# Optimization experiments

Measured on AMD Instinct MI355X. Metric: run time of the kernel, lower is better.

Reference implementation:

```python
import jax, jax.numpy as jnp
import numpy as np

B, DIM, H, W = 4, 512, 64, 64
NH = 8
HD = DIM // NH  # 64
CS = 16         # TTT mini_batch_size
BASE_LR = 1.0
EPS_IN = 1e-6   # inner ttt LayerNorm / post_norm eps
EPS_OUT = 1e-5  # wrapper nn.LayerNorm eps


def _ln(x, g, b, eps):
    mu = x.mean(-1, keepdims=True)
    var = ((x - mu) ** 2).mean(-1, keepdims=True)
    return (x - mu) / jnp.sqrt(var + eps) * g + b


def _ln_l2_bwd(Z, tgt, g, b):
    # fused: d/dZ of 0.5*||LN(Z; g,b) - tgt||^2
    D = Z.shape[-1]
    mu = Z.mean(-1, keepdims=True)
    var = ((Z - mu) ** 2).mean(-1, keepdims=True)
    std = jnp.sqrt(var + EPS_IN)
    xh = (Z - mu) / std
    gxh = ((g * xh + b) - tgt) * g
    return (D * gxh - gxh.sum(-1, keepdims=True) - xh * (gxh * xh).sum(-1, keepdims=True)) / (D * std)


def _rope(x, L):
    # x: [B, nh, L, f], llama-style rotary, theta=10000
    inv = 1.0 / (10000.0 ** (jnp.arange(0, HD, 2, dtype=jnp.float32) / HD))
    fr = jnp.arange(L, dtype=jnp.float32)[:, None] * inv[None, :]
    emb = jnp.concatenate([fr, fr], axis=-1)  # [L, f]
    cos, sin = jnp.cos(emb), jnp.sin(emb)
    x1, x2 = jnp.split(x, 2, axis=-1)
    return x * cos + jnp.concatenate([-x2, x1], axis=-1) * sin


def setup_inputs() -> dict:
    key = jax.random.key(0)
    ks = jax.random.split(key, 8)
    r = lambda k, s: 0.02 * jax.random.normal(k, s, dtype=jnp.float32)
    return {
        "x": jax.random.normal(ks[0], (B, DIM, H, W), dtype=jnp.float32),
        "ln_w": jnp.ones((DIM,), jnp.float32), "ln_b": jnp.zeros((DIM,), jnp.float32),
        "q_w": r(ks[1], (DIM, DIM)), "k_w": r(ks[2], (DIM, DIM)),
        "v_w": r(ks[3], (DIM, DIM)), "o_w": r(ks[4], (DIM, DIM)),
        "W1": r(ks[5], (NH, HD, HD)), "b1": jnp.zeros((NH, 1, HD), jnp.float32),
        "ttt_ln_w": jnp.ones((NH, HD), jnp.float32), "ttt_ln_b": jnp.zeros((NH, HD), jnp.float32),
        "lr_w": r(ks[6], (NH, 1, DIM)), "lr_b": jnp.zeros((NH, 1, 1), jnp.float32),
        "tok_idx_delta": jnp.zeros((CS,), jnp.float32),
        "post_w": jnp.ones((DIM,), jnp.float32), "post_b": jnp.zeros((DIM,), jnp.float32),
    }


def _ttt_linear(xn, q_w, k_w, v_w, o_w, W1, b1, ttt_ln_w, ttt_ln_b, lr_w, lr_b, tok_idx_delta, post_w, post_b):
    Bsz, L, _ = xn.shape
    NC = L // CS
    heads = lambda t: t.reshape(Bsz, L, NH, HD).transpose(0, 2, 1, 3)  # [B,nh,L,f]
    XQ = _rope(heads(xn @ q_w.T), L)
    XK = _rope(heads(xn @ k_w.T), L)
    XV = heads(xn @ v_w.T)

    # per-token learning rates eta: [B,nh,NC,CS,CS]
    Xc = xn.reshape(Bsz, NC, CS, DIM)
    ttt_lr = jax.nn.sigmoid(jnp.einsum("bnkc,hdc->bhnkd", Xc, lr_w) + lr_b.reshape(1, NH, 1, 1, 1))
    ttt_lr_eta = (BASE_LR / HD) * ttt_lr.transpose(0, 1, 2, 4, 3)  # [B,nh,NC,1,CS]
    token_idx = jnp.maximum(1.0 / jnp.arange(1, CS + 1, dtype=jnp.float32) + tok_idx_delta, 0.0)
    eta = token_idx.reshape(1, 1, 1, CS, 1) * ttt_lr_eta  # [B,nh,NC,CS,CS]

    g = ttt_ln_w[None, :, None, :]   # [1,nh,1,f]
    bb = ttt_ln_b[None, :, None, :]

    def step(carry, inp):
        W1c, b1c = carry                       # [B,nh,f,f], [B,nh,1,f]
        xq, xk, xv, et = inp                   # [B,nh,CS,f], eta [B,nh,CS,CS]
        Z1 = xk @ W1c + b1c
        grad = _ln_l2_bwd(Z1, xv - xk, g, bb)  # [B,nh,CS,f]
        Attn1 = jnp.tril(xq @ xk.swapaxes(-1, -2))
        b1_bar = b1c - jnp.tril(et) @ grad
        Z1_bar = xq @ W1c - (et * Attn1) @ grad + b1_bar
        last_eta = et[..., -1, :, None]        # [B,nh,CS,1]
        W1n = W1c - (last_eta * xk).swapaxes(-1, -2) @ grad
        b1n = b1c - (last_eta * grad).sum(-2, keepdims=True)
        return (W1n, b1n), xq + _ln(Z1_bar, g, bb, EPS_IN)

    W1_0 = jnp.broadcast_to(W1[None], (Bsz, NH, HD, HD)) + 0.0
    b1_0 = jnp.broadcast_to(b1[None], (Bsz, NH, 1, HD)) + 0.0
    chunk = lambda t: t.reshape(Bsz, NH, NC, CS, HD).transpose(2, 0, 1, 3, 4)
    _, out = jax.lax.scan(step, (W1_0, b1_0),
                          (chunk(XQ), chunk(XK), chunk(XV), eta.transpose(2, 0, 1, 3, 4)))
    # [NC,B,nh,CS,f] -> [B,L,D]
    out = out.transpose(1, 2, 0, 3, 4).reshape(Bsz, NH, L, HD).transpose(0, 2, 1, 3).reshape(Bsz, L, DIM)
    return _ln(out, post_w, post_b, EPS_IN) @ o_w.T


def reference(x, ln_w, ln_b, q_w, k_w, v_w, o_w, W1, b1, ttt_ln_w, ttt_ln_b, lr_w, lr_b, tok_idx_delta, post_w, post_b):
    Bsz, d = x.shape[:2]
    n_tok = x.shape[2] * x.shape[3]
    xf = x.reshape(Bsz, d, n_tok).transpose(0, 2, 1)   # [B, L, D]
    xn = _ln(xf, ln_w, ln_b, EPS_OUT)
    y = _ttt_linear(xn, q_w, k_w, v_w, o_w, W1, b1, ttt_ln_w, ttt_ln_b, lr_w, lr_b, tok_idx_delta, post_w, post_b)
    return y.transpose(0, 2, 1).reshape(x.shape)
```

## Files before the change

kernel.cpp:

```cpp
#include <hip/hip_runtime.h>
#include <hip/hip_bf16.h>
#include <math.h>

#define L_TOK 4096
#define DIMC  512

static __device__ __forceinline__ float4 f4fma(float a, const float4 b, const float4 c) {
    return make_float4(fmaf(a, b.x, c.x), fmaf(a, b.y, c.y), fmaf(a, b.z, c.z), fmaf(a, b.w, c.w));
}

__global__ __launch_bounds__(256) void rope_table_kernel(float* __restrict__ ctab, float* __restrict__ stab) {
    int idx = blockIdx.x * 256 + threadIdx.x;
    if (idx >= L_TOK * 32) return;
    int t = idx >> 5, m = idx & 31;
    float inv = 1.0f / powf(10000.0f, (float)(2 * m) * (1.0f / 64.0f));
    float fr = (float)t * inv;
    ctab[idx] = cosf(fr);
    stab[idx] = sinf(fr);
}

__global__ __launch_bounds__(256) void ln_in_kernel(const float* __restrict__ x,
                                                    const float* __restrict__ w,
                                                    const float* __restrict__ bia,
                                                    float* __restrict__ xn) {
    __shared__ float tile[16][516];
    __shared__ float redA[4][16], redB[4][16];
    __shared__ float mu_s[16], rs_s[16];
    int blk = blockIdx.x;
    int b = blk >> 8;
    int t0 = (blk & 255) << 4;
    int tid = threadIdx.x;
    int tt = tid & 15, cg = tid >> 4;
    int wid = tid >> 6;
    const float* xp = x + (size_t)b * DIMC * L_TOK + t0 + tt;
    float sum = 0.0f, sq = 0.0f;
#pragma unroll
    for (int i = 0; i < 32; i++) {
        int c = cg + (i << 4);
        float v = xp[(size_t)c * L_TOK];
        tile[tt][c] = v;
        sum += v; sq += v * v;
    }
    sum += __shfl_xor(sum, 16); sum += __shfl_xor(sum, 32);
    sq  += __shfl_xor(sq, 16);  sq  += __shfl_xor(sq, 32);
    if ((tid & 63) < 16) { redA[wid][tt] = sum; redB[wid][tt] = sq; }
    __syncthreads();
    if (tid < 16) {
        float s = redA[0][tid] + redA[1][tid] + redA[2][tid] + redA[3][tid];
        float q = redB[0][tid] + redB[1][tid] + redB[2][tid] + redB[3][tid];
        float mu = s * (1.0f / 512.0f);
        mu_s[tid] = mu;
        rs_s[tid] = rsqrtf(q * (1.0f / 512.0f) - mu * mu + 1e-5f);
    }
    __syncthreads();
    int half = tid >> 7;
    int cc = (tid & 127) << 2;
    float4 wv = *(const float4*)&w[cc];
    float4 bv = *(const float4*)&bia[cc];
    float* xnp = xn + ((size_t)b * L_TOK + t0) * DIMC;
#pragma unroll
    for (int i = 0; i < 8; i++) {
        int rr = half + (i << 1);
        float mu = mu_s[rr], rs = rs_s[rr];
        float4 v = *(float4*)&tile[rr][cc];
        float4 o;
        o.x = fmaf((v.x - mu) * rs, wv.x, bv.x);
        o.y = fmaf((v.y - mu) * rs, wv.y, bv.y);
        o.z = fmaf((v.z - mu) * rs, wv.z, bv.z);
        o.w = fmaf((v.w - mu) * rs, wv.w, bv.w);
        *(float4*)&xnp[(size_t)rr * DIMC + cc] = o;
    }
}

__global__ __launch_bounds__(256) void lr_kernel(const float* __restrict__ xn,
                                                 const float* __restrict__ lrw,
                                                 const float* __restrict__ lrb,
                                                 float* __restrict__ lre) {
    int tid = threadIdx.x;
    int lane = tid & 63, wid = tid >> 6;
    int tok = blockIdx.x * 4 + wid;
    const float* xp = xn + (size_t)tok * DIMC + lane * 8;
    float4 a0 = *(const float4*)xp;
    float4 a1 = *(const float4*)(xp + 4);
    int bb = tok >> 12, t = tok & 4095;
#pragma unroll
    for (int h = 0; h < 8; h++) {
        const float* wp = lrw + h * DIMC + lane * 8;
        float4 w0 = *(const float4*)wp;
        float4 w1 = *(const float4*)(wp + 4);
        float s = a0.x * w0.x + a0.y * w0.y + a0.z * w0.z + a0.w * w0.w
                + a1.x * w1.x + a1.y * w1.y + a1.z * w1.z + a1.w * w1.w;
        s += __shfl_xor(s, 1); s += __shfl_xor(s, 2); s += __shfl_xor(s, 4);
        s += __shfl_xor(s, 8); s += __shfl_xor(s, 16); s += __shfl_xor(s, 32);
        if (lane == 0) {
            float v = s + lrb[h];
            lre[(size_t)(bb * 8 + h) * L_TOK + t] = (1.0f / 64.0f) / (1.0f + expf(-v));
        }
    }
}

__global__ __launch_bounds__(256) void qkv_gemm_kernel(const float* __restrict__ A,
                                                       const float* __restrict__ qw,
                                                       const float* __restrict__ kw,
                                                       const float* __restrict__ vw,
                                                       float* __restrict__ XQ,
                                                       float* __restrict__ XK,
                                                       float* __restrict__ XV) {
    __shared__ float As[16][68];
    __shared__ float Bs[16][68];
    int tid = threadIdx.x;
    int mt = blockIdx.x, nt = blockIdx.y;
    const float* wsel = (nt < 8) ? qw : (nt < 16) ? kw : vw;
    int h = nt & 7;
    int lrow = tid >> 2, lk = (tid & 3) << 2;
    int tm = tid >> 4, tn = tid & 15;
    float acc[4][4] = {};
    const float* ap = A + (size_t)(mt * 64 + lrow) * DIMC + lk;
    const float* bp = wsel + (size_t)(h * 64 + lrow) * DIMC + lk;
    for (int k0 = 0; k0 < DIMC; k0 += 16) {
        float4 av = *(const float4*)(ap + k0);
        float4 bv = *(const float4*)(bp + k0);
        As[lk + 0][lrow] = av.x; As[lk + 1][lrow] = av.y; As[lk + 2][lrow] = av.z; As[lk + 3][lrow] = av.w;
        Bs[lk + 0][lrow] = bv.x; Bs[lk + 1][lrow] = bv.y; Bs[lk + 2][lrow] = bv.z; Bs[lk + 3][lrow] = bv.w;
        __syncthreads();
#pragma unroll
        for (int kk = 0; kk < 16; kk++) {
            float4 a = *(const float4*)&As[kk][tm << 2];
            float4 bq = *(const float4*)&Bs[kk][tn << 2];
            float aa[4] = {a.x, a.y, a.z, a.w};
            float bb[4] = {bq.x, bq.y, bq.z, bq.w};
#pragma unroll
            for (int i = 0; i < 4; i++)
#pragma unroll
                for (int j = 0; j < 4; j++)
                    acc[i][j] = fmaf(aa[i], bb[j], acc[i][j]);
        }
        __syncthreads();
    }
    int m0 = mt * 64 + (tm << 2);
    int bb2 = m0 >> 12, t = m0 & 4095;
    float* dst = (nt < 8) ? XQ : (nt < 16) ? XK : XV;
    dst += ((size_t)(bb2 * 8 + h) * L_TOK + t) * 64 + (tn << 2);
#pragma unroll
    for (int i = 0; i < 4; i++)
        *(float4*)(dst + (size_t)i * 64) = make_float4(acc[i][0], acc[i][1], acc[i][2], acc[i][3]);
}

__global__ __launch_bounds__(256) void rope_kernel(float* __restrict__ XQ, float* __restrict__ XK,
                                                   const float* __restrict__ ctab,
                                                   const float* __restrict__ stab) {
    int idx = blockIdx.x * 256 + threadIdx.x;
    int d = idx & 31;
    int t = (idx >> 5) & 4095;
    int bh = (idx >> 17) & 31;
    int tensor = idx >> 22;
    float* p = (tensor ? XK : XQ) + ((size_t)bh * L_TOK + t) * 64;
    float c = ctab[(t << 5) + d], s = stab[(t << 5) + d];
    float x1 = p[d], x2 = p[d + 32];
    p[d] = x1 * c - x2 * s;
    p[d + 32] = x2 * c + x1 * s;
}

__global__ __launch_bounds__(256) void scan_kernel(const float* __restrict__ XQ,
                                                   const float* __restrict__ XK,
                                                   const float* __restrict__ XV,
                                                   const float* __restrict__ lre,
                                                   const float* __restrict__ tok_delta,
                                                   const float* __restrict__ W1i,
                                                   const float* __restrict__ b1i,
                                                   const float* __restrict__ tw,
                                                   const float* __restrict__ tb,
                                                   float* __restrict__ attn_out) {
    __shared__ float W1[64][64];
    __shared__ float b1v[64];
    __shared__ float xqs[2][16][68], xks[2][16][68], xvs[2][16][68];
    __shared__ float grads[16][68];
    __shared__ float etas[2][16];
    __shared__ float coefC[16][16];
    __shared__ float sj[16];
    int tid = threadIdx.x;
    int r = tid >> 4, dq = tid & 15, d0 = dq << 2;
    int bh = blockIdx.x, h = bh & 7, b = bh >> 3;
#pragma unroll
    for (int i = 0; i < 4; i++) {
        int c = r + (i << 4);
        *(float4*)&W1[c][d0] = *(const float4*)&W1i[(size_t)h * 4096 + c * 64 + d0];
    }
    if (r == 0) *(float4*)&b1v[d0] = *(const float4*)&b1i[h * 64 + d0];
    float4 gw = *(const float4*)&tw[h * 64 + d0];
    float4 bw = *(const float4*)&tb[h * 64 + d0];
    float tok_r = fmaxf(1.0f / (float)(r + 1) + tok_delta[r], 0.0f);
    float tok15 = fmaxf(1.0f / 16.0f + tok_delta[15], 0.0f);
    const size_t base = (size_t)bh * L_TOK * 64;
    {
        size_t off = base + (size_t)r * 64 + d0;
        *(float4*)&xqs[0][r][d0] = *(const float4*)(XQ + off);
        *(float4*)&xks[0][r][d0] = *(const float4*)(XK + off);
        *(float4*)&xvs[0][r][d0] = *(const float4*)(XV + off);
        if (tid < 16) etas[0][tid] = lre[(size_t)bh * L_TOK + tid];
    }
    __syncthreads();
    int cur = 0;
    for (int n = 0; n < 256; n++) {
        int np = (n < 255) ? n + 1 : 255;
        size_t poff = base + (size_t)np * 1024 + (size_t)r * 64 + d0;
        float4 pfq = *(const float4*)(XQ + poff);
        float4 pfk = *(const float4*)(XK + poff);
        float4 pfv = *(const float4*)(XV + poff);
        float pfe = 0.0f;
        if (tid < 16) pfe = lre[(size_t)bh * L_TOK + np * 16 + tid];

        float4 z = *(float4*)&b1v[d0];
        float att = 0.0f;
#pragma unroll
        for (int c4 = 0; c4 < 16; c4++) {
            int c = c4 << 2;
            float4 xkr = *(float4*)&xks[cur][r][c];
            float4 xqr = *(float4*)&xqs[cur][r][c];
            float4 xkq = *(float4*)&xks[cur][dq][c];
            att += xqr.x * xkq.x + xqr.y * xkq.y + xqr.z * xkq.z + xqr.w * xkq.w;
            z = f4fma(xkr.x, *(float4*)&W1[c + 0][d0], z);
            z = f4fma(xkr.y, *(float4*)&W1[c + 1][d0], z);
            z = f4fma(xkr.z, *(float4*)&W1[c + 2][d0], z);
            z = f4fma(xkr.w, *(float4*)&W1[c + 3][d0], z);
        }
        float s = z.x + z.y + z.z + z.w;
        s += __shfl_xor(s, 1); s += __shfl_xor(s, 2); s += __shfl_xor(s, 4); s += __shfl_xor(s, 8);
        float mu = s * (1.0f / 64.0f);
        float4 dz = make_float4(z.x - mu, z.y - mu, z.z - mu, z.w - mu);
        float q = dz.x * dz.x + dz.y * dz.y + dz.z * dz.z + dz.w * dz.w;
        q += __shfl_xor(q, 1); q += __shfl_xor(q, 2); q += __shfl_xor(q, 4); q += __shfl_xor(q, 8);
        float rstd = rsqrtf(q * (1.0f / 64.0f) + 1e-6f);
        float4 xh = make_float4(dz.x * rstd, dz.y * rstd, dz.z * rstd, dz.w * rstd);
        float4 xvv = *(float4*)&xvs[cur][r][d0];
        float4 xkk = *(float4*)&xks[cur][r][d0];
        float4 gxh;
        gxh.x = (fmaf(gw.x, xh.x, bw.x) - (xvv.x - xkk.x)) * gw.x;
        gxh.y = (fmaf(gw.y, xh.y, bw.y) - (xvv.y - xkk.y)) * gw.y;
        gxh.z = (fmaf(gw.z, xh.z, bw.z) - (xvv.z - xkk.z)) * gw.z;
        gxh.w = (fmaf(gw.w, xh.w, bw.w) - (xvv.w - xkk.w)) * gw.w;
        float s1 = gxh.x + gxh.y + gxh.z + gxh.w;
        s1 += __shfl_xor(s1, 1); s1 += __shfl_xor(s1, 2); s1 += __shfl_xor(s1, 4); s1 += __shfl_xor(s1, 8);
        float s2 = gxh.x * xh.x + gxh.y * xh.y + gxh.z * xh.z + gxh.w * xh.w;
        s2 += __shfl_xor(s2, 1); s2 += __shfl_xor(s2, 2); s2 += __shfl_xor(s2, 4); s2 += __shfl_xor(s2, 8);
        float cgr = rstd * (1.0f / 64.0f);
        float4 grad;
        grad.x = (64.0f * gxh.x - s1 - xh.x * s2) * cgr;
        grad.y = (64.0f * gxh.y - s1 - xh.y * s2) * cgr;
        grad.z = (64.0f * gxh.z - s1 - xh.z * s2) * cgr;
        grad.w = (64.0f * gxh.w - s1 - xh.w * s2) * cgr;
        *(float4*)&grads[r][d0] = grad;
        float ceta = etas[cur][dq];
        coefC[r][dq] = (dq <= r) ? tok_r * ceta * (1.0f + att) : 0.0f;
        if (r == 15) sj[dq] = tok15 * ceta;
        __syncthreads();

        float4 z2 = *(float4*)&b1v[d0];
#pragma unroll
        for (int c4 = 0; c4 < 16; c4++) {
            int c = c4 << 2;
            float4 xqr = *(float4*)&xqs[cur][r][c];
            z2 = f4fma(xqr.x, *(float4*)&W1[c + 0][d0], z2);
            z2 = f4fma(xqr.y, *(float4*)&W1[c + 1][d0], z2);
            z2 = f4fma(xqr.z, *(float4*)&W1[c + 2][d0], z2);
            z2 = f4fma(xqr.w, *(float4*)&W1[c + 3][d0], z2);
        }
#pragma unroll
        for (int j = 0; j < 16; j++) {
            float cj = coefC[r][j];
            float4 gj = *(float4*)&grads[j][d0];
            z2 = f4fma(-cj, gj, z2);
        }
        float so = z2.x + z2.y + z2.z + z2.w;
        so += __shfl_xor(so, 1); so += __shfl_xor(so, 2); so += __shfl_xor(so, 4); so += __shfl_xor(so, 8);
        float mu2 = so * (1.0f / 64.0f);
        float4 dz2 = make_float4(z2.x - mu2, z2.y - mu2, z2.z - mu2, z2.w - mu2);
        float q2 = dz2.x * dz2.x + dz2.y * dz2.y + dz2.z * dz2.z + dz2.w * dz2.w;
        q2 += __shfl_xor(q2, 1); q2 += __shfl_xor(q2, 2); q2 += __shfl_xor(q2, 4); q2 += __shfl_xor(q2, 8);
        float rstd2 = rsqrtf(q2 * (1.0f / 64.0f) + 1e-6f);
        float4 xq4 = *(float4*)&xqs[cur][r][d0];
        float4 o;
        o.x = fmaf(dz2.x * rstd2, gw.x, bw.x) + xq4.x;
        o.y = fmaf(dz2.y * rstd2, gw.y, bw.y) + xq4.y;
        o.z = fmaf(dz2.z * rstd2, gw.z, bw.z) + xq4.z;
        o.w = fmaf(dz2.w * rstd2, gw.w, bw.w) + xq4.w;
        *(float4*)(attn_out + ((size_t)b * L_TOK + (size_t)n * 16 + r) * DIMC + h * 64 + d0) = o;
        __syncthreads();

        float4 acc0 = make_float4(0, 0, 0, 0), acc1 = acc0, acc2 = acc0, acc3 = acc0;
#pragma unroll
        for (int j = 0; j < 16; j++) {
            float sjj = sj[j];
            float4 gj = *(float4*)&grads[j][d0];
            acc0 = f4fma(sjj * xks[cur][j][r],      gj, acc0);
            acc1 = f4fma(sjj * xks[cur][j][r + 16], gj, acc1);
            acc2 = f4fma(sjj * xks[cur][j][r + 32], gj, acc2);
            acc3 = f4fma(sjj * xks[cur][j][r + 48], gj, acc3);
        }
        {
            float4 w0 = *(float4*)&W1[r][d0];
            w0.x -= acc0.x; w0.y -= acc0.y; w0.z -= acc0.z; w0.w -= acc0.w;
            *(float4*)&W1[r][d0] = w0;
            float4 w1 = *(float4*)&W1[r + 16][d0];
            w1.x -= acc1.x; w1.y -= acc1.y; w1.z -= acc1.z; w1.w -= acc1.w;
            *(float4*)&W1[r + 16][d0] = w1;
            float4 w2 = *(float4*)&W1[r + 32][d0];
            w2.x -= acc2.x; w2.y -= acc2.y; w2.z -= acc2.z; w2.w -= acc2.w;
            *(float4*)&W1[r + 32][d0] = w2;
            float4 w3 = *(float4*)&W1[r + 48][d0];
            w3.x -= acc3.x; w3.y -= acc3.y; w3.z -= acc3.z; w3.w -= acc3.w;
            *(float4*)&W1[r + 48][d0] = w3;
        }
        if (r == 0) {
            float4 ab = make_float4(0, 0, 0, 0);
#pragma unroll
            for (int j = 0; j < 16; j++)
                ab = f4fma(sj[j], *(float4*)&grads[j][d0], ab);
            float4 bv = *(float4*)&b1v[d0];
            bv.x -= ab.x; bv.y -= ab.y; bv.z -= ab.z; bv.w -= ab.w;
            *(float4*)&b1v[d0] = bv;
        }
        *(float4*)&xqs[cur ^ 1][r][d0] = pfq;
        *(float4*)&xks[cur ^ 1][r][d0] = pfk;
        *(float4*)&xvs[cur ^ 1][r][d0] = pfv;
        if (tid < 16) etas[cur ^ 1][tid] = pfe;
        __syncthreads();
        cur ^= 1;
    }
}

__global__ __launch_bounds__(256) void post_ln_kernel(float* __restrict__ at,
                                                      const float* __restrict__ w,
                                                      const float* __restrict__ b) {
    __shared__ float redA[4], redB[4];
    int row = blockIdx.x, tid = threadIdx.x;
    float* p = at + (size_t)row * DIMC;
    float v0 = p[tid], v1 = p[tid + 256];
    float s = v0 + v1, q = v0 * v0 + v1 * v1;
    s += __shfl_xor(s, 1); s += __shfl_xor(s, 2); s += __shfl_xor(s, 4);
    s += __shfl_xor(s, 8); s += __shfl_xor(s, 16); s += __shfl_xor(s, 32);
    q += __shfl_xor(q, 1); q += __shfl_xor(q, 2); q += __shfl_xor(q, 4);
    q += __shfl_xor(q, 8); q += __shfl_xor(q, 16); q += __shfl_xor(q, 32);
    if ((tid & 63) == 0) { redA[tid >> 6] = s; redB[tid >> 6] = q; }
    __syncthreads();
    s = redA[0] + redA[1] + redA[2] + redA[3];
    q = redB[0] + redB[1] + redB[2] + redB[3];
    float mu = s * (1.0f / 512.0f);
    float rs = rsqrtf(q * (1.0f / 512.0f) - mu * mu + 1e-6f);
    p[tid]       = fmaf((v0 - mu) * rs, w[tid],       b[tid]);
    p[tid + 256] = fmaf((v1 - mu) * rs, w[tid + 256], b[tid + 256]);
}

__global__ __launch_bounds__(256) void out_gemm_kernel(const float* __restrict__ A,
                                                       const float* __restrict__ ow,
                                                       float* __restrict__ out) {
    __shared__ float As[16][68];
    __shared__ float Bs[16][68];
    int tid = threadIdx.x;
    int mt = blockIdx.x, nt = blockIdx.y;
    int lrow = tid >> 2, lk = (tid & 3) << 2;
    int tm = tid >> 4, tn = tid & 15;
    float acc[4][4] = {};
    const float* ap = A + (size_t)(mt * 64 + lrow) * DIMC + lk;
    const float* bp = ow + (size_t)(nt * 64 + lrow) * DIMC + lk;
    for (int k0 = 0; k0 < DIMC; k0 += 16) {
        float4 av = *(const float4*)(ap + k0);
        float4 bv = *(const float4*)(bp + k0);
        As[lk + 0][lrow] = av.x; As[lk + 1][lrow] = av.y; As[lk + 2][lrow] = av.z; As[lk + 3][lrow] = av.w;
        Bs[lk + 0][lrow] = bv.x; Bs[lk + 1][lrow] = bv.y; Bs[lk + 2][lrow] = bv.z; Bs[lk + 3][lrow] = bv.w;
        __syncthreads();
#pragma unroll
        for (int kk = 0; kk < 16; kk++) {
            float4 a = *(const float4*)&As[kk][tm << 2];
            float4 bq = *(const float4*)&Bs[kk][tn << 2];
            float aa[4] = {a.x, a.y, a.z, a.w};
            float bb[4] = {bq.x, bq.y, bq.z, bq.w};
#pragma unroll
            for (int i = 0; i < 4; i++)
#pragma unroll
                for (int j = 0; j < 4; j++)
                    acc[i][j] = fmaf(aa[i], bb[j], acc[i][j]);
        }
        __syncthreads();
    }
    int m0 = mt * 64 + (tm << 2);
    int bb2 = m0 >> 12, t = m0 & 4095;
    int n0 = nt * 64 + (tn << 2);
#pragma unroll
    for (int j = 0; j < 4; j++)
        *(float4*)(out + ((size_t)(bb2 * DIMC) + n0 + j) * L_TOK + t) =
            make_float4(acc[0][j], acc[1][j], acc[2][j], acc[3][j]);
}

extern "C" void kernel_launch(void* const* d_in, const int* in_sizes, int n_in,
                              void* d_out, int out_size, void* d_ws, size_t ws_size,
                              hipStream_t stream) {
    (void)in_sizes; (void)n_in; (void)out_size; (void)ws_size;
    const float* x       = (const float*)d_in[0];
    const float* ln_w    = (const float*)d_in[1];
    const float* ln_b    = (const float*)d_in[2];
    const float* q_w     = (const float*)d_in[3];
    const float* k_w     = (const float*)d_in[4];
    const float* v_w     = (const float*)d_in[5];
    const float* o_w     = (const float*)d_in[6];
    const float* W1      = (const float*)d_in[7];
    const float* b1      = (const float*)d_in[8];
    const float* ttt_w   = (const float*)d_in[9];
    const float* ttt_b   = (const float*)d_in[10];
    const float* lr_w    = (const float*)d_in[11];
    const float* lr_b    = (const float*)d_in[12];
    const float* tok_d   = (const float*)d_in[13];
    const float* post_w  = (const float*)d_in[14];
    const float* post_b  = (const float*)d_in[15];

    float* ws = (float*)d_ws;
    const size_t NTD = (size_t)4 * L_TOK * DIMC;
    float* xn   = ws;
    float* XQb  = ws + NTD;
    float* XKb  = ws + 2 * NTD;
    float* XVb  = (float*)d_out;
    float* lre  = ws + 3 * NTD;
    float* ctab = lre + 131072;
    float* stab = ctab + 131072;
    float* attn = xn;

    rope_table_kernel<<<512, 256, 0, stream>>>(ctab, stab);
    ln_in_kernel<<<1024, 256, 0, stream>>>(x, ln_w, ln_b, xn);
    lr_kernel<<<4096, 256, 0, stream>>>(xn, lr_w, lr_b, lre);
    {
        dim3 g(256, 24);
        qkv_gemm_kernel<<<g, 256, 0, stream>>>(xn, q_w, k_w, v_w, XQb, XKb, XVb);
    }
    rope_kernel<<<32768, 256, 0, stream>>>(XQb, XKb, ctab, stab);
    scan_kernel<<<32, 256, 0, stream>>>(XQb, XKb, XVb, lre, tok_d, W1, b1, ttt_w, ttt_b, attn);
    post_ln_kernel<<<16384, 256, 0, stream>>>(attn, post_w, post_b);
    {
        dim3 g(256, 8);
        out_gemm_kernel<<<g, 256, 0, stream>>>(attn, o_w, (float*)d_out);
    }
}
```

Baseline: 1.760 ms.

## Double-buffer TTT weights in scan to drop a barrier; enlarge QKV GEMM tile

The scan kernel now keeps two copies of W1 and b1 in shared memory, writing the update into the next buffer. This removes one block barrier per chunk and merges the weight-update loop with the output loop. The query projection through W1 is computed in the same pass as the key projection, so W1 is read from shared memory once instead of twice, and each thread keeps its own 4-row slice of W1 in registers for the update. Separately, the QKV GEMM tile grows from 64 to 128 rows per block with 8x4 per-thread accumulators, raising register use and shared memory per block.

```diff
diff --git a/kernel.cpp b/kernel.cpp
--- a/kernel.cpp
+++ b/kernel.cpp
@@ -106,43 +106,47 @@
                                                        float* __restrict__ XQ,
                                                        float* __restrict__ XK,
                                                        float* __restrict__ XV) {
-    __shared__ float As[16][68];
+    __shared__ float As[16][136];
     __shared__ float Bs[16][68];
     int tid = threadIdx.x;
     int mt = blockIdx.x, nt = blockIdx.y;
     const float* wsel = (nt < 8) ? qw : (nt < 16) ? kw : vw;
     int h = nt & 7;
-    int lrow = tid >> 2, lk = (tid & 3) << 2;
-    int tm = tid >> 4, tn = tid & 15;
-    float acc[4][4] = {};
-    const float* ap = A + (size_t)(mt * 64 + lrow) * DIMC + lk;
-    const float* bp = wsel + (size_t)(h * 64 + lrow) * DIMC + lk;
+    int arow = tid >> 1, ak = (tid & 1) << 3;
+    int brow = tid >> 2, bk = (tid & 3) << 2;
+    int tm8 = (tid >> 4) << 3, tn = tid & 15;
+    float acc[8][4] = {};
+    const float* ap = A + (size_t)(mt * 128 + arow) * DIMC + ak;
+    const float* bp = wsel + (size_t)(h * 64 + brow) * DIMC + bk;
     for (int k0 = 0; k0 < DIMC; k0 += 16) {
-        float4 av = *(const float4*)(ap + k0);
+        float4 a0 = *(const float4*)(ap + k0);
+        float4 a1 = *(const float4*)(ap + k0 + 4);
         float4 bv = *(const float4*)(bp + k0);
-        As[lk + 0][lrow] = av.x; As[lk + 1][lrow] = av.y; As[lk + 2][lrow] = av.z; As[lk + 3][lrow] = av.w;
-        Bs[lk + 0][lrow] = bv.x; Bs[lk + 1][lrow] = bv.y; Bs[lk + 2][lrow] = bv.z; Bs[lk + 3][lrow] = bv.w;
+        As[ak + 0][arow] = a0.x; As[ak + 1][arow] = a0.y; As[ak + 2][arow] = a0.z; As[ak + 3][arow] = a0.w;
+        As[ak + 4][arow] = a1.x; As[ak + 5][arow] = a1.y; As[ak + 6][arow] = a1.z; As[ak + 7][arow] = a1.w;
+        Bs[bk + 0][brow] = bv.x; Bs[bk + 1][brow] = bv.y; Bs[bk + 2][brow] = bv.z; Bs[bk + 3][brow] = bv.w;
         __syncthreads();
 #pragma unroll
         for (int kk = 0; kk < 16; kk++) {
-            float4 a = *(const float4*)&As[kk][tm << 2];
-            float4 bq = *(const float4*)&Bs[kk][tn << 2];
-            float aa[4] = {a.x, a.y, a.z, a.w};
-            float bb[4] = {bq.x, bq.y, bq.z, bq.w};
-#pragma unroll
-            for (int i = 0; i < 4; i++)
+            float4 va0 = *(const float4*)&As[kk][tm8];
+            float4 va1 = *(const float4*)&As[kk][tm8 + 4];
+            float4 vb  = *(const float4*)&Bs[kk][tn << 2];
+            float aa[8] = {va0.x, va0.y, va0.z, va0.w, va1.x, va1.y, va1.z, va1.w};
+            float bb[4] = {vb.x, vb.y, vb.z, vb.w};
+#pragma unroll
+            for (int i = 0; i < 8; i++)
 #pragma unroll
                 for (int j = 0; j < 4; j++)
                     acc[i][j] = fmaf(aa[i], bb[j], acc[i][j]);
         }
         __syncthreads();
     }
-    int m0 = mt * 64 + (tm << 2);
+    int m0 = mt * 128 + tm8;
     int bb2 = m0 >> 12, t = m0 & 4095;
     float* dst = (nt < 8) ? XQ : (nt < 16) ? XK : XV;
     dst += ((size_t)(bb2 * 8 + h) * L_TOK + t) * 64 + (tn << 2);
 #pragma unroll
-    for (int i = 0; i < 4; i++)
+    for (int i = 0; i < 8; i++)
         *(float4*)(dst + (size_t)i * 64) = make_float4(acc[i][0], acc[i][1], acc[i][2], acc[i][3]);
 }
 
@@ -171,12 +175,12 @@
                                                    const float* __restrict__ tw,
                                                    const float* __restrict__ tb,
                                                    float* __restrict__ attn_out) {
-    __shared__ float W1[64][64];
-    __shared__ float b1v[64];
+    __shared__ float W1d[2][64][64];
+    __shared__ float b1d[2][64];
     __shared__ float xqs[2][16][68], xks[2][16][68], xvs[2][16][68];
     __shared__ float grads[16][68];
     __shared__ float etas[2][16];
-    __shared__ float coefC[16][16];
+    __shared__ float coefC[16][17];
     __shared__ float sj[16];
     int tid = threadIdx.x;
     int r = tid >> 4, dq = tid & 15, d0 = dq << 2;
@@ -184,9 +188,9 @@
 #pragma unroll
     for (int i = 0; i < 4; i++) {
         int c = r + (i << 4);
-        *(float4*)&W1[c][d0] = *(const float4*)&W1i[(size_t)h * 4096 + c * 64 + d0];
-    }
-    if (r == 0) *(float4*)&b1v[d0] = *(const float4*)&b1i[h * 64 + d0];
+        *(float4*)&W1d[0][c][d0] = *(const float4*)&W1i[(size_t)h * 4096 + c * 64 + d0];
+    }
+    if (r == 0) *(float4*)&b1d[0][d0] = *(const float4*)&b1i[h * 64 + d0];
     float4 gw = *(const float4*)&tw[h * 64 + d0];
     float4 bw = *(const float4*)&tb[h * 64 + d0];
     float tok_r = fmaxf(1.0f / (float)(r + 1) + tok_delta[r], 0.0f);
@@ -210,19 +214,28 @@
         float pfe = 0.0f;
         if (tid < 16) pfe = lre[(size_t)bh * L_TOK + np * 16 + tid];
 
-        float4 z = *(float4*)&b1v[d0];
+        float4 b1reg = *(float4*)&b1d[cur][d0];
+        float4 z  = b1reg;
+        float4 z2 = b1reg;
         float att = 0.0f;
+        float4 wc0, wc1, wc2, wc3;
+        wc0 = wc1 = wc2 = wc3 = make_float4(0, 0, 0, 0);
 #pragma unroll
         for (int c4 = 0; c4 < 16; c4++) {
             int c = c4 << 2;
             float4 xkr = *(float4*)&xks[cur][r][c];
             float4 xqr = *(float4*)&xqs[cur][r][c];
             float4 xkq = *(float4*)&xks[cur][dq][c];
+            float4 w0 = *(float4*)&W1d[cur][c + 0][d0];
+            float4 w1 = *(float4*)&W1d[cur][c + 1][d0];
+            float4 w2 = *(float4*)&W1d[cur][c + 2][d0];
+            float4 w3 = *(float4*)&W1d[cur][c + 3][d0];
             att += xqr.x * xkq.x + xqr.y * xkq.y + xqr.z * xkq.z + xqr.w * xkq.w;
-            z = f4fma(xkr.x, *(float4*)&W1[c + 0][d0], z);
-            z = f4fma(xkr.y, *(float4*)&W1[c + 1][d0], z);
-            z = f4fma(xkr.z, *(float4*)&W1[c + 2][d0], z);
-            z = f4fma(xkr.w, *(float4*)&W1[c + 3][d0], z);
+            z  = f4fma(xkr.x, w0, z);  z  = f4fma(xkr.y, w1, z);
+            z  = f4fma(xkr.z, w2, z);  z  = f4fma(xkr.w, w3, z);
+            z2 = f4fma(xqr.x, w0, z2); z2 = f4fma(xqr.y, w1, z2);
+            z2 = f4fma(xqr.z, w2, z2); z2 = f4fma(xqr.w, w3, z2);
+            if (c4 == r) { wc0 = w0; wc1 = w1; wc2 = w2; wc3 = w3; }
         }
         float s = z.x + z.y + z.z + z.w;
         s += __shfl_xor(s, 1); s += __shfl_xor(s, 2); s += __shfl_xor(s, 4); s += __shfl_xor(s, 8);
@@ -255,21 +268,20 @@
         if (r == 15) sj[dq] = tok15 * ceta;
         __syncthreads();
 
-        float4 z2 = *(float4*)&b1v[d0];
-#pragma unroll
-        for (int c4 = 0; c4 < 16; c4++) {
-            int c = c4 << 2;
-            float4 xqr = *(float4*)&xqs[cur][r][c];
-            z2 = f4fma(xqr.x, *(float4*)&W1[c + 0][d0], z2);
-            z2 = f4fma(xqr.y, *(float4*)&W1[c + 1][d0], z2);
-            z2 = f4fma(xqr.z, *(float4*)&W1[c + 2][d0], z2);
-            z2 = f4fma(xqr.w, *(float4*)&W1[c + 3][d0], z2);
-        }
+        int r4 = r << 2;
+        float4 acc0 = make_float4(0, 0, 0, 0), acc1 = acc0, acc2 = acc0, acc3 = acc0, accb = acc0;
 #pragma unroll
         for (int j = 0; j < 16; j++) {
+            float4 gj = *(float4*)&grads[j][d0];
             float cj = coefC[r][j];
-            float4 gj = *(float4*)&grads[j][d0];
+            float sjj = sj[j];
+            float4 xk4 = *(float4*)&xks[cur][j][r4];
             z2 = f4fma(-cj, gj, z2);
+            acc0 = f4fma(sjj * xk4.x, gj, acc0);
+            acc1 = f4fma(sjj * xk4.y, gj, acc1);
+            acc2 = f4fma(sjj * xk4.z, gj, acc2);
+            acc3 = f4fma(sjj * xk4.w, gj, acc3);
+            accb = f4fma(sjj, gj, accb);
         }
         float so = z2.x + z2.y + z2.z + z2.w;
         so += __shfl_xor(so, 1); so += __shfl_xor(so, 2); so += __shfl_xor(so, 4); so += __shfl_xor(so, 8);
@@ -285,45 +297,18 @@
         o.z = fmaf(dz2.z * rstd2, gw.z, bw.z) + xq4.z;
         o.w = fmaf(dz2.w * rstd2, gw.w, bw.w) + xq4.w;
         *(float4*)(attn_out + ((size_t)b * L_TOK + (size_t)n * 16 + r) * DIMC + h * 64 + d0) = o;
-        __syncthreads();
-
-        float4 acc0 = make_float4(0, 0, 0, 0), acc1 = acc0, acc2 = acc0, acc3 = acc0;
-#pragma unroll
-        for (int j = 0; j < 16; j++) {
-            float sjj = sj[j];
-            float4 gj = *(float4*)&grads[j][d0];
-            acc0 = f4fma(sjj * xks[cur][j][r],      gj, acc0);
-            acc1 = f4fma(sjj * xks[cur][j][r + 16], gj, acc1);
-            acc2 = f4fma(sjj * xks[cur][j][r + 32], gj, acc2);
-            acc3 = f4fma(sjj * xks[cur][j][r + 48], gj, acc3);
-        }
-        {
-            float4 w0 = *(float4*)&W1[r][d0];
-            w0.x -= acc0.x; w0.y -= acc0.y; w0.z -= acc0.z; w0.w -= acc0.w;
-            *(float4*)&W1[r][d0] = w0;
-            float4 w1 = *(float4*)&W1[r + 16][d0];
-            w1.x -= acc1.x; w1.y -= acc1.y; w1.z -= acc1.z; w1.w -= acc1.w;
-            *(float4*)&W1[r + 16][d0] = w1;
-            float4 w2 = *(float4*)&W1[r + 32][d0];
-            w2.x -= acc2.x; w2.y -= acc2.y; w2.z -= acc2.z; w2.w -= acc2.w;
-            *(float4*)&W1[r + 32][d0] = w2;
-            float4 w3 = *(float4*)&W1[r + 48][d0];
-            w3.x -= acc3.x; w3.y -= acc3.y; w3.z -= acc3.z; w3.w -= acc3.w;
-            *(float4*)&W1[r + 48][d0] = w3;
-        }
-        if (r == 0) {
-            float4 ab = make_float4(0, 0, 0, 0);
-#pragma unroll
-            for (int j = 0; j < 16; j++)
-                ab = f4fma(sj[j], *(float4*)&grads[j][d0], ab);
-            float4 bv = *(float4*)&b1v[d0];
-            bv.x -= ab.x; bv.y -= ab.y; bv.z -= ab.z; bv.w -= ab.w;
-            *(float4*)&b1v[d0] = bv;
-        }
-        *(float4*)&xqs[cur ^ 1][r][d0] = pfq;
-        *(float4*)&xks[cur ^ 1][r][d0] = pfk;
-        *(float4*)&xvs[cur ^ 1][r][d0] = pfv;
-        if (tid < 16) etas[cur ^ 1][tid] = pfe;
+
+        int nxt = cur ^ 1;
+        *(float4*)&W1d[nxt][r4 + 0][d0] = make_float4(wc0.x - acc0.x, wc0.y - acc0.y, wc0.z - acc0.z, wc0.w - acc0.w);
+        *(float4*)&W1d[nxt][r4 + 1][d0] = make_float4(wc1.x - acc1.x, wc1.y - acc1.y, wc1.z - acc1.z, wc1.w - acc1.w);
+        *(float4*)&W1d[nxt][r4 + 2][d0] = make_float4(wc2.x - acc2.x, wc2.y - acc2.y, wc2.z - acc2.z, wc2.w - acc2.w);
+        *(float4*)&W1d[nxt][r4 + 3][d0] = make_float4(wc3.x - acc3.x, wc3.y - acc3.y, wc3.z - acc3.z, wc3.w - acc3.w);
+        if (r == 0)
+            *(float4*)&b1d[nxt][d0] = make_float4(b1reg.x - accb.x, b1reg.y - accb.y, b1reg.z - accb.z, b1reg.w - accb.w);
+        *(float4*)&xqs[nxt][r][d0] = pfq;
+        *(float4*)&xks[nxt][r][d0] = pfk;
+        *(float4*)&xvs[nxt][r][d0] = pfv;
+        if (tid < 16) etas[nxt][tid] = pfe;
         __syncthreads();
         cur ^= 1;
     }
@@ -428,7 +413,7 @@
     ln_in_kernel<<<1024, 256, 0, stream>>>(x, ln_w, ln_b, xn);
     lr_kernel<<<4096, 256, 0, stream>>>(xn, lr_w, lr_b, lre);
     {
-        dim3 g(256, 24);
+        dim3 g(128, 24);
         qkv_gemm_kernel<<<g, 256, 0, stream>>>(xn, q_w, k_w, v_w, XQb, XKb, XVb);
     }
     rope_kernel<<<32768, 256, 0, stream>>>(XQb, XKb, ctab, stab);
```

After: 2.213 ms. +25.7%, slower.
